# Kernel optimization log

Measured on AMD Instinct MI355X. Metric: run time of the kernel, lower is better.

Reference implementation:

```python
import jax, jax.numpy as jnp
import numpy as np
from jax import lax

NUM_STATES = 16
NUM_CHAINS = 2
NUM_NODES = 2000
NUM_ITERS = 1000


def setup_inputs() -> dict:
    key = jax.random.key(0)
    k0, k1, k2, k3 = jax.random.split(key, 4)
    return {
        "unnormalized_state_init": jax.random.normal(k0, (NUM_STATES,), dtype=jnp.float32),
        "unnormalized_chain_weights": jax.random.normal(k1, (NUM_STATES, NUM_CHAINS), dtype=jnp.float32),
        "unnormalized_emission_matrix": jax.random.normal(k2, (NUM_STATES, NUM_NODES), dtype=jnp.float32),
        "unnormalized_transition_matrix": jax.random.normal(k3, (NUM_STATES, NUM_STATES), dtype=jnp.float32),
    }


def reference(unnormalized_state_init, unnormalized_chain_weights,
              unnormalized_emission_matrix, unnormalized_transition_matrix):
    # Normalize parameters in log domain (matches torch log_softmax dims)
    log_state_init = jax.nn.log_softmax(unnormalized_state_init, axis=0)            # (S,)
    log_chain_weights = jax.nn.log_softmax(unnormalized_chain_weights, axis=1)      # (S,C)
    log_emission_matrix = jax.nn.log_softmax(unnormalized_emission_matrix, axis=1)  # (S,N)
    log_transition_matrix = jax.nn.log_softmax(unnormalized_transition_matrix, axis=1)  # (S,S)

    # Sequential HMM forward recursion in log domain:
    # h_t[j] = logsumexp_i( h_{t-1}[i] + log_T[i, j] )
    def step(h, _):
        h_next = jax.nn.logsumexp(h[:, None] + log_transition_matrix, axis=0)
        return h_next, h_next

    _, hs = lax.scan(step, log_state_init, None, length=NUM_ITERS - 1)
    log_hidden_state_probs = jnp.concatenate([log_state_init[None, :], hs], axis=0)  # (T,S)

    # P(node | state, chain, iter) joint in log domain: (T,S,C,N)
    # (original repeats emission across the 2 chains; here broadcast over C)
    log_observed_state_probs_ = (
        log_emission_matrix[None, :, None, :]
        + log_chain_weights[None, :, :, None]
        + log_hidden_state_probs[:, :, None, None]
    )
    # Marginalize states then chains (logsumexp over axes 1 then 1 == axes (1,2))
    log_observed_state_probs = jax.nn.logsumexp(log_observed_state_probs_, axis=(1, 2))  # (T,N)
    return log_observed_state_probs
```

## Files before the change

kernel.cpp:

```cpp
#include <hip/hip_runtime.h>
#include <hip/hip_bf16.h>
#include <math.h>

#define NS 16
#define NN 2000
#define NT 1000

#define WS_E 0
#define WS_P 32000

__global__ __launch_bounds__(256) void prep_kernel(
    const float* __restrict__ init,
    const float* __restrict__ trans,
    const float* __restrict__ emis,
    float* __restrict__ ws)
{
  const int tid = threadIdx.x;
  const int b = blockIdx.x;

  if (b > 0) {
    __shared__ float red[256];
    const int s = b - 1;
    const float* row = emis + s * NN;
    float m = -1e30f;
    for (int n = tid; n < NN; n += 256) m = fmaxf(m, row[n]);
    red[tid] = m; __syncthreads();
    for (int off = 128; off > 0; off >>= 1) {
      if (tid < off) red[tid] = fmaxf(red[tid], red[tid + off]);
      __syncthreads();
    }
    m = red[0];
    __syncthreads();
    float sm = 0.f;
    for (int n = tid; n < NN; n += 256) sm += __expf(row[n] - m);
    red[tid] = sm; __syncthreads();
    for (int off = 128; off > 0; off >>= 1) {
      if (tid < off) red[tid] += red[tid + off];
      __syncthreads();
    }
    const float lse = m + __logf(red[0]);
    for (int n = tid; n < NN; n += 256)
      ws[WS_E + s * NN + n] = __expf(row[n] - lse);
    return;
  }

  __shared__ float Tp[16][16];
  __shared__ float A[16][16];
  __shared__ float T32[16][16];
  __shared__ float C[32][16];
  __shared__ float p0v[16];

  const int i = tid >> 4, j = tid & 15;

  A[i][j] = trans[tid];
  __syncthreads();
  float m = -1e30f;
  #pragma unroll
  for (int k = 0; k < 16; ++k) m = fmaxf(m, A[i][k]);
  float sm = 0.f;
  #pragma unroll
  for (int k = 0; k < 16; ++k) sm += __expf(A[i][k] - m);
  const float tp = __expf(A[i][j] - m) / sm;

  if (tid < 16) {
    float m2 = -1e30f, s2 = 0.f;
    #pragma unroll
    for (int k = 0; k < 16; ++k) m2 = fmaxf(m2, init[k]);
    #pragma unroll
    for (int k = 0; k < 16; ++k) s2 += __expf(init[k] - m2);
    p0v[tid] = __expf(init[tid] - m2) / s2;
  }
  __syncthreads();
  Tp[i][j] = tp;
  A[i][j]  = tp;
  __syncthreads();

  for (int q = 0; q < 5; ++q) {
    float acc = 0.f;
    #pragma unroll
    for (int k = 0; k < 16; ++k) acc += A[i][k] * A[k][j];
    __syncthreads();
    A[i][j] = acc;
    __syncthreads();
  }
  T32[i][j] = A[i][j];
  if (tid < 16) C[0][tid] = p0v[tid];
  A[i][j] = (i == j) ? 1.f : 0.f;
  __syncthreads();

  for (int q = 1; q < 32; ++q) {
    float c = 0.f;
    if (tid < 16) {
      #pragma unroll
      for (int k = 0; k < 16; ++k) c += C[q - 1][k] * T32[k][tid];
    }
    __syncthreads();
    if (tid < 16) C[q][tid] = c;
    __syncthreads();
  }

  for (int r = 0; r < 32; ++r) {
    float v0 = 0.f, v1 = 0.f;
    #pragma unroll
    for (int k = 0; k < 16; ++k) {
      const float a = A[k][j];
      v0 += C[i][k] * a;
      v1 += C[i + 16][k] * a;
    }
    ws[WS_P + (i * 32 + r) * 16 + j]        = v0;
    ws[WS_P + ((i + 16) * 32 + r) * 16 + j] = v1;

    float acc = 0.f;
    #pragma unroll
    for (int k = 0; k < 16; ++k) acc += A[i][k] * Tp[k][j];
    __syncthreads();
    A[i][j] = acc;
    __syncthreads();
  }
}

__global__ __launch_bounds__(256) void out_kernel(
    const float* __restrict__ ws, float* __restrict__ out)
{
  const int tid = threadIdx.x;
  const int n0 = blockIdx.x * 1024 + tid * 4;
  if (n0 + 3 >= NN) return;
  const int tbase = blockIdx.y * 4;

  float4 e[16];
  #pragma unroll
  for (int s = 0; s < 16; ++s)
    e[s] = *(const float4*)(ws + WS_E + s * NN + n0);

  #pragma unroll
  for (int tt = 0; tt < 4; ++tt) {
    const int t = tbase + tt;
    const float* Pr = ws + WS_P + t * 16;
    float4 acc = make_float4(0.f, 0.f, 0.f, 0.f);
    #pragma unroll
    for (int s = 0; s < 16; ++s) {
      const float p = Pr[s];
      acc.x += p * e[s].x;
      acc.y += p * e[s].y;
      acc.z += p * e[s].z;
      acc.w += p * e[s].w;
    }
    float4 o;
    o.x = __logf(acc.x);
    o.y = __logf(acc.y);
    o.z = __logf(acc.z);
    o.w = __logf(acc.w);
    *(float4*)(out + t * NN + n0) = o;
  }
}

extern "C" void kernel_launch(void* const* d_in, const int* in_sizes, int n_in,
                              void* d_out, int out_size, void* d_ws, size_t ws_size,
                              hipStream_t stream) {
  const float* init  = (const float*)d_in[0];
  const float* emis  = (const float*)d_in[2];
  const float* trans = (const float*)d_in[3];
  float* ws  = (float*)d_ws;
  float* out = (float*)d_out;

  hipLaunchKernelGGL(prep_kernel, dim3(17), dim3(256), 0, stream,
                     init, trans, emis, ws);
  hipLaunchKernelGGL(out_kernel, dim3(2, 250), dim3(256), 0, stream, ws, out);
}
```

Measured before the change: 85.39 us.

## Fuse prep and output kernels into one with per-block matrix power

Replaces the two-kernel pipeline (a serial prep block computing 1000 state distributions plus emission softmax into workspace, then the output kernel) with a single kernel of 250 blocks. Each block redundantly normalizes the emission rows, computes T^(4*blockIdx) by binary exponentiation of 16x16 matrices, and derives its own four time-step distributions before writing output. This removes the serial 32-step prep chain, the workspace round trip and one launch, at the cost of redundant per-block emission reductions and exps. It also drops the max subtraction in the emission softmax, which risks overflow for large inputs.

Measured after the change: 72.92 us. 1.17x faster.

```diff
diff --git a/kernel.cpp b/kernel.cpp
--- a/kernel.cpp
+++ b/kernel.cpp
@@ -1,156 +1,140 @@
 #include <hip/hip_runtime.h>
-#include <hip/hip_bf16.h>
 #include <math.h>
 
-#define NS 16
 #define NN 2000
-#define NT 1000
+#define NG 500
 
-#define WS_E 0
-#define WS_P 32000
+__global__ __launch_bounds__(256) void ssm_fused(
+    const float* __restrict__ init,
+    const float* __restrict__ emis,
+    const float* __restrict__ trans,
+    float* __restrict__ out)
+{
+  __shared__ float Tp[16][16];
+  __shared__ float Bm[16][16];
+  __shared__ float Rm[16][16];
+  __shared__ float p0v[16];
+  __shared__ float sumExp[16];
+  __shared__ float w[4][16];
+  __shared__ float wd[4][16];
 
-__global__ __launch_bounds__(256) void prep_kernel(
-    const float* __restrict__ init,
-    const float* __restrict__ trans,
-    const float* __restrict__ emis,
-    float* __restrict__ ws)
-{
-  const int tid = threadIdx.x;
-  const int b = blockIdx.x;
+  const int tid  = threadIdx.x;
+  const int i    = tid >> 4, j = tid & 15;
+  const int lane = tid & 63, wv = tid >> 6;
 
-  if (b > 0) {
-    __shared__ float red[256];
-    const int s = b - 1;
-    const float* row = emis + s * NN;
-    float m = -1e30f;
-    for (int n = tid; n < NN; n += 256) m = fmaxf(m, row[n]);
-    red[tid] = m; __syncthreads();
-    for (int off = 128; off > 0; off >>= 1) {
-      if (tid < off) red[tid] = fmaxf(red[tid], red[tid + off]);
-      __syncthreads();
+  Bm[i][j] = trans[tid];
+
+  float ssum[4] = {0.f, 0.f, 0.f, 0.f};
+  for (int g = lane; g < NG; g += 64) {
+    #pragma unroll
+    for (int si = 0; si < 4; ++si) {
+      const int s = wv * 4 + si;
+      float4 v = *(const float4*)(emis + s * NN + g * 4);
+      ssum[si] += __expf(v.x) + __expf(v.y) + __expf(v.z) + __expf(v.w);
     }
-    m = red[0];
-    __syncthreads();
-    float sm = 0.f;
-    for (int n = tid; n < NN; n += 256) sm += __expf(row[n] - m);
-    red[tid] = sm; __syncthreads();
-    for (int off = 128; off > 0; off >>= 1) {
-      if (tid < off) red[tid] += red[tid + off];
-      __syncthreads();
-    }
-    const float lse = m + __logf(red[0]);
-    for (int n = tid; n < NN; n += 256)
-      ws[WS_E + s * NN + n] = __expf(row[n] - lse);
-    return;
+  }
+  #pragma unroll
+  for (int si = 0; si < 4; ++si) {
+    float v = ssum[si];
+    #pragma unroll
+    for (int off = 32; off > 0; off >>= 1) v += __shfl_down(v, off);
+    if (lane == 0) sumExp[wv * 4 + si] = v;
   }
 
-  __shared__ float Tp[16][16];
-  __shared__ float A[16][16];
-  __shared__ float T32[16][16];
-  __shared__ float C[32][16];
-  __shared__ float p0v[16];
-
-  const int i = tid >> 4, j = tid & 15;
-
-  A[i][j] = trans[tid];
-  __syncthreads();
-  float m = -1e30f;
-  #pragma unroll
-  for (int k = 0; k < 16; ++k) m = fmaxf(m, A[i][k]);
-  float sm = 0.f;
-  #pragma unroll
-  for (int k = 0; k < 16; ++k) sm += __expf(A[i][k] - m);
-  const float tp = __expf(A[i][j] - m) / sm;
-
   if (tid < 16) {
-    float m2 = -1e30f, s2 = 0.f;
+    float m = -1e30f, s2 = 0.f;
     #pragma unroll
-    for (int k = 0; k < 16; ++k) m2 = fmaxf(m2, init[k]);
+    for (int k = 0; k < 16; ++k) m = fmaxf(m, init[k]);
     #pragma unroll
-    for (int k = 0; k < 16; ++k) s2 += __expf(init[k] - m2);
-    p0v[tid] = __expf(init[tid] - m2) / s2;
+    for (int k = 0; k < 16; ++k) s2 += __expf(init[k] - m);
+    p0v[tid] = __expf(init[tid] - m) / s2;
   }
   __syncthreads();
-  Tp[i][j] = tp;
-  A[i][j]  = tp;
+
+  {
+    float m = -1e30f;
+    #pragma unroll
+    for (int k = 0; k < 16; ++k) m = fmaxf(m, Bm[i][k]);
+    float sm = 0.f;
+    #pragma unroll
+    for (int k = 0; k < 16; ++k) sm += __expf(Bm[i][k] - m);
+    const float tp = __expf(Bm[i][j] - m) / sm;
+    __syncthreads();
+    Tp[i][j] = tp;
+    Bm[i][j] = tp;
+    Rm[i][j] = (i == j) ? 1.f : 0.f;
+  }
   __syncthreads();
 
-  for (int q = 0; q < 5; ++q) {
+  #pragma unroll
+  for (int q = 0; q < 2; ++q) {
     float acc = 0.f;
     #pragma unroll
-    for (int k = 0; k < 16; ++k) acc += A[i][k] * A[k][j];
+    for (int k = 0; k < 16; ++k) acc += Bm[i][k] * Bm[k][j];
     __syncthreads();
-    A[i][j] = acc;
-    __syncthreads();
-  }
-  T32[i][j] = A[i][j];
-  if (tid < 16) C[0][tid] = p0v[tid];
-  A[i][j] = (i == j) ? 1.f : 0.f;
-  __syncthreads();
-
-  for (int q = 1; q < 32; ++q) {
-    float c = 0.f;
-    if (tid < 16) {
-      #pragma unroll
-      for (int k = 0; k < 16; ++k) c += C[q - 1][k] * T32[k][tid];
-    }
-    __syncthreads();
-    if (tid < 16) C[q][tid] = c;
+    Bm[i][j] = acc;
     __syncthreads();
   }
 
-  for (int r = 0; r < 32; ++r) {
-    float v0 = 0.f, v1 = 0.f;
+  int e = blockIdx.x;
+  while (e) {
+    const bool mul = (e & 1);
+    float accR = 0.f, accB = 0.f;
+    if (mul) {
+      #pragma unroll
+      for (int k = 0; k < 16; ++k) accR += Rm[i][k] * Bm[k][j];
+    }
     #pragma unroll
-    for (int k = 0; k < 16; ++k) {
-      const float a = A[k][j];
-      v0 += C[i][k] * a;
-      v1 += C[i + 16][k] * a;
-    }
-    ws[WS_P + (i * 32 + r) * 16 + j]        = v0;
-    ws[WS_P + ((i + 16) * 32 + r) * 16 + j] = v1;
+    for (int k = 0; k < 16; ++k) accB += Bm[i][k] * Bm[k][j];
+    __syncthreads();
+    if (mul) Rm[i][j] = accR;
+    Bm[i][j] = accB;
+    __syncthreads();
+    e >>= 1;
+  }
 
+  if (tid < 16) {
     float acc = 0.f;
     #pragma unroll
-    for (int k = 0; k < 16; ++k) acc += A[i][k] * Tp[k][j];
-    __syncthreads();
-    A[i][j] = acc;
+    for (int k = 0; k < 16; ++k) acc += p0v[k] * Rm[k][tid];
+    w[0][tid] = acc;
+  }
+  __syncthreads();
+  for (int tt = 1; tt < 4; ++tt) {
+    if (tid < 16) {
+      float acc = 0.f;
+      #pragma unroll
+      for (int k = 0; k < 16; ++k) acc += w[tt - 1][k] * Tp[k][tid];
+      w[tt][tid] = acc;
+    }
     __syncthreads();
   }
-}
+  if (tid < 64) wd[tid >> 4][tid & 15] = w[tid >> 4][tid & 15] / sumExp[tid & 15];
+  __syncthreads();
 
-__global__ __launch_bounds__(256) void out_kernel(
-    const float* __restrict__ ws, float* __restrict__ out)
-{
-  const int tid = threadIdx.x;
-  const int n0 = blockIdx.x * 1024 + tid * 4;
-  if (n0 + 3 >= NN) return;
-  const int tbase = blockIdx.y * 4;
-
-  float4 e[16];
-  #pragma unroll
-  for (int s = 0; s < 16; ++s)
-    e[s] = *(const float4*)(ws + WS_E + s * NN + n0);
-
-  #pragma unroll
-  for (int tt = 0; tt < 4; ++tt) {
-    const int t = tbase + tt;
-    const float* Pr = ws + WS_P + t * 16;
-    float4 acc = make_float4(0.f, 0.f, 0.f, 0.f);
+  const int tbase = blockIdx.x * 4;
+  for (int g = tid; g < NG; g += 256) {
+    float4 ex[16];
     #pragma unroll
     for (int s = 0; s < 16; ++s) {
-      const float p = Pr[s];
-      acc.x += p * e[s].x;
-      acc.y += p * e[s].y;
-      acc.z += p * e[s].z;
-      acc.w += p * e[s].w;
+      float4 v = *(const float4*)(emis + s * NN + g * 4);
+      ex[s].x = __expf(v.x); ex[s].y = __expf(v.y);
+      ex[s].z = __expf(v.z); ex[s].w = __expf(v.w);
     }
-    float4 o;
-    o.x = __logf(acc.x);
-    o.y = __logf(acc.y);
-    o.z = __logf(acc.z);
-    o.w = __logf(acc.w);
-    *(float4*)(out + t * NN + n0) = o;
+    #pragma unroll
+    for (int tt = 0; tt < 4; ++tt) {
+      float4 acc = make_float4(0.f, 0.f, 0.f, 0.f);
+      #pragma unroll
+      for (int s = 0; s < 16; ++s) {
+        const float p = wd[tt][s];
+        acc.x += p * ex[s].x; acc.y += p * ex[s].y;
+        acc.z += p * ex[s].z; acc.w += p * ex[s].w;
+      }
+      float4 o;
+      o.x = __logf(acc.x); o.y = __logf(acc.y);
+      o.z = __logf(acc.z); o.w = __logf(acc.w);
+      *(float4*)(out + (tbase + tt) * NN + g * 4) = o;
+    }
   }
 }
 
@@ -160,10 +144,8 @@
   const float* init  = (const float*)d_in[0];
   const float* emis  = (const float*)d_in[2];
   const float* trans = (const float*)d_in[3];
-  float* ws  = (float*)d_ws;
   float* out = (float*)d_out;
 
-  hipLaunchKernelGGL(prep_kernel, dim3(17), dim3(256), 0, stream,
-                     init, trans, emis, ws);
-  hipLaunchKernelGGL(out_kernel, dim3(2, 250), dim3(256), 0, stream, ws, out);
+  hipLaunchKernelGGL(ssm_fused, dim3(250), dim3(256), 0, stream,
+                     init, emis, trans, out);
 }
```

## Replace serial transition-power chains with doubling scheme in prep kernel

Applied to the files above, without the earlier changes.

The prep block now computes the hidden-state probabilities with repeated squaring. It keeps T^1..T^16, builds the 32 block-start vectors in log2 steps, and fills each block of 32 by doubling, instead of running two serial 31/32-step chains of 16x16 matmuls with barriers. The emission softmax drops the max pass and one read pass by exponentiating float4-loaded values directly. This shortens the serial critical path of the single prep block. The risk is overflow or inexactness in the emission softmax when inputs are large.

New measurement: 85.46 us. About the same (+0.1%).

```diff
diff --git a/kernel.cpp b/kernel.cpp
--- a/kernel.cpp
+++ b/kernel.cpp
@@ -1,11 +1,7 @@
 #include <hip/hip_runtime.h>
-#include <hip/hip_bf16.h>
 #include <math.h>
 
-#define NS 16
 #define NN 2000
-#define NT 1000
-
 #define WS_E 0
 #define WS_P 32000
 
@@ -15,53 +11,47 @@
     const float* __restrict__ emis,
     float* __restrict__ ws)
 {
+  __shared__ float red[256];
+  __shared__ float Tpw[5][16][16];
+  __shared__ float M[16][16];
+  __shared__ float C[32][16];
+  __shared__ float p0v[16];
+
   const int tid = threadIdx.x;
   const int b = blockIdx.x;
 
   if (b > 0) {
-    __shared__ float red[256];
     const int s = b - 1;
-    const float* row = emis + s * NN;
-    float m = -1e30f;
-    for (int n = tid; n < NN; n += 256) m = fmaxf(m, row[n]);
-    red[tid] = m; __syncthreads();
-    for (int off = 128; off > 0; off >>= 1) {
-      if (tid < off) red[tid] = fmaxf(red[tid], red[tid + off]);
-      __syncthreads();
+    const float4* rin = (const float4*)(emis + s * NN);
+    float4* rout = (float4*)(ws + WS_E + s * NN);
+    const bool has2 = (tid + 256) < 500;
+    float4 v0 = rin[tid];
+    float4 v1 = has2 ? rin[tid + 256] : make_float4(0.f, 0.f, 0.f, 0.f);
+    float4 e0, e1;
+    e0.x = __expf(v0.x); e0.y = __expf(v0.y); e0.z = __expf(v0.z); e0.w = __expf(v0.w);
+    float sm = e0.x + e0.y + e0.z + e0.w;
+    if (has2) {
+      e1.x = __expf(v1.x); e1.y = __expf(v1.y); e1.z = __expf(v1.z); e1.w = __expf(v1.w);
+      sm += e1.x + e1.y + e1.z + e1.w;
     }
-    m = red[0];
-    __syncthreads();
-    float sm = 0.f;
-    for (int n = tid; n < NN; n += 256) sm += __expf(row[n] - m);
     red[tid] = sm; __syncthreads();
     for (int off = 128; off > 0; off >>= 1) {
       if (tid < off) red[tid] += red[tid + off];
       __syncthreads();
     }
-    const float lse = m + __logf(red[0]);
-    for (int n = tid; n < NN; n += 256)
-      ws[WS_E + s * NN + n] = __expf(row[n] - lse);
+    const float inv = 1.f / red[0];
+    e0.x *= inv; e0.y *= inv; e0.z *= inv; e0.w *= inv;
+    rout[tid] = e0;
+    if (has2) {
+      e1.x *= inv; e1.y *= inv; e1.z *= inv; e1.w *= inv;
+      rout[tid + 256] = e1;
+    }
     return;
   }
 
-  __shared__ float Tp[16][16];
-  __shared__ float A[16][16];
-  __shared__ float T32[16][16];
-  __shared__ float C[32][16];
-  __shared__ float p0v[16];
-
   const int i = tid >> 4, j = tid & 15;
 
-  A[i][j] = trans[tid];
-  __syncthreads();
-  float m = -1e30f;
-  #pragma unroll
-  for (int k = 0; k < 16; ++k) m = fmaxf(m, A[i][k]);
-  float sm = 0.f;
-  #pragma unroll
-  for (int k = 0; k < 16; ++k) sm += __expf(A[i][k] - m);
-  const float tp = __expf(A[i][j] - m) / sm;
-
+  M[i][j] = trans[tid];
   if (tid < 16) {
     float m2 = -1e30f, s2 = 0.f;
     #pragma unroll
@@ -71,50 +61,75 @@
     p0v[tid] = __expf(init[tid] - m2) / s2;
   }
   __syncthreads();
-  Tp[i][j] = tp;
-  A[i][j]  = tp;
+
+  {
+    float m = -1e30f;
+    #pragma unroll
+    for (int k = 0; k < 16; ++k) m = fmaxf(m, M[i][k]);
+    float sm = 0.f;
+    #pragma unroll
+    for (int k = 0; k < 16; ++k) sm += __expf(M[i][k] - m);
+    const float tp = __expf(M[i][j] - m) / sm;
+    __syncthreads();
+    Tpw[0][i][j] = tp;
+  }
   __syncthreads();
 
-  for (int q = 0; q < 5; ++q) {
+  #pragma unroll
+  for (int e = 0; e < 4; ++e) {
     float acc = 0.f;
     #pragma unroll
-    for (int k = 0; k < 16; ++k) acc += A[i][k] * A[k][j];
-    __syncthreads();
-    A[i][j] = acc;
+    for (int k = 0; k < 16; ++k) acc += Tpw[e][i][k] * Tpw[e][k][j];
+    Tpw[e + 1][i][j] = acc;
     __syncthreads();
   }
-  T32[i][j] = A[i][j];
+  {
+    float acc = 0.f;
+    #pragma unroll
+    for (int k = 0; k < 16; ++k) acc += Tpw[4][i][k] * Tpw[4][k][j];
+    M[i][j] = acc;
+  }
   if (tid < 16) C[0][tid] = p0v[tid];
-  A[i][j] = (i == j) ? 1.f : 0.f;
   __syncthreads();
 
-  for (int q = 1; q < 32; ++q) {
-    float c = 0.f;
-    if (tid < 16) {
+  #pragma unroll
+  for (int s = 0; s < 5; ++s) {
+    const int k = 1 << s;
+    const bool active = (tid < k * 16);
+    float accC = 0.f, accM = 0.f;
+    if (active) {
       #pragma unroll
-      for (int k = 0; k < 16; ++k) c += C[q - 1][k] * T32[k][tid];
+      for (int kk = 0; kk < 16; ++kk) accC += C[i][kk] * M[kk][j];
+    }
+    if (s < 4) {
+      #pragma unroll
+      for (int kk = 0; kk < 16; ++kk) accM += M[i][kk] * M[kk][j];
     }
     __syncthreads();
-    if (tid < 16) C[q][tid] = c;
+    if (active) C[k + i][j] = accC;
+    if (s < 4) M[i][j] = accM;
     __syncthreads();
   }
 
-  for (int r = 0; r < 32; ++r) {
-    float v0 = 0.f, v1 = 0.f;
-    #pragma unroll
-    for (int k = 0; k < 16; ++k) {
-      const float a = A[k][j];
-      v0 += C[i][k] * a;
-      v1 += C[i + 16][k] * a;
+  float* Pg = ws + WS_P;
+  for (int x = tid; x < 32 * 16; x += 256)
+    Pg[(x >> 4) * 32 * 16 + (x & 15)] = C[x >> 4][x & 15];
+  __syncthreads();
+
+  #pragma unroll
+  for (int e = 0; e < 5; ++e) {
+    const int d = 1 << e;
+    const int total = 32 * d * 16;
+    for (int x = tid; x < total; x += 256) {
+      const int rr = x >> 4, jj = x & 15;
+      const int q = rr >> e;
+      const int r = d + (rr & (d - 1));
+      const float* src = Pg + (32 * q + r - d) * 16;
+      float acc = 0.f;
+      #pragma unroll
+      for (int kk = 0; kk < 16; ++kk) acc += src[kk] * Tpw[e][kk][jj];
+      Pg[(32 * q + r) * 16 + jj] = acc;
     }
-    ws[WS_P + (i * 32 + r) * 16 + j]        = v0;
-    ws[WS_P + ((i + 16) * 32 + r) * 16 + j] = v1;
-
-    float acc = 0.f;
-    #pragma unroll
-    for (int k = 0; k < 16; ++k) acc += A[i][k] * Tp[k][j];
-    __syncthreads();
-    A[i][j] = acc;
     __syncthreads();
   }
 }
@@ -134,23 +149,18 @@
 
   #pragma unroll
   for (int tt = 0; tt < 4; ++tt) {
-    const int t = tbase + tt;
-    const float* Pr = ws + WS_P + t * 16;
+    const float* Pr = ws + WS_P + (tbase + tt) * 16;
     float4 acc = make_float4(0.f, 0.f, 0.f, 0.f);
     #pragma unroll
     for (int s = 0; s < 16; ++s) {
       const float p = Pr[s];
-      acc.x += p * e[s].x;
-      acc.y += p * e[s].y;
-      acc.z += p * e[s].z;
-      acc.w += p * e[s].w;
+      acc.x += p * e[s].x; acc.y += p * e[s].y;
+      acc.z += p * e[s].z; acc.w += p * e[s].w;
     }
     float4 o;
-    o.x = __logf(acc.x);
-    o.y = __logf(acc.y);
-    o.z = __logf(acc.z);
-    o.w = __logf(acc.w);
-    *(float4*)(out + t * NN + n0) = o;
+    o.x = __logf(acc.x); o.y = __logf(acc.y);
+    o.z = __logf(acc.z); o.w = __logf(acc.w);
+    *(float4*)(out + (tbase + tt) * NN + n0) = o;
   }
 }
 
```
